# Optimization experiments

Measured on AMD Instinct MI355X. Metric: run time of the kernel, lower is better.

Reference implementation:

```python
import jax, jax.numpy as jnp
import numpy as np

HEAD_DIM = 128
ATTN_PAD_SEQ_LEN = 64
NUM_REQ = 128
NUM_HEAD = 32


def setup_inputs() -> dict:
    key = jax.random.key(0)
    qkv = jax.random.normal(key, (NUM_REQ, ATTN_PAD_SEQ_LEN, NUM_HEAD, HEAD_DIM * 3), dtype=jnp.float32)
    return {"qkv": qkv, "kv_seq_len": 64}


def reference(qkv, kv_seq_len):
    # qkv: [B, S, H, 3*D] packed Q|K|V along last dim
    q, k, v = jnp.split(qkv, 3, axis=-1)  # each [B, S, H, D]
    scale = 1.0 / jnp.sqrt(jnp.asarray(HEAD_DIM, dtype=qkv.dtype))
    # scores: [B, H, Sq, Sk]
    scores = jnp.einsum('bqhd,bkhd->bhqk', q, k) * scale
    # mask out padded KV positions beyond the active kv length
    kv_mask = jnp.arange(ATTN_PAD_SEQ_LEN) < kv_seq_len  # [Sk]
    scores = jnp.where(kv_mask[None, None, None, :], scores, jnp.asarray(-jnp.inf, dtype=scores.dtype))
    attn = jax.nn.softmax(scores, axis=-1)
    out = jnp.einsum('bhqk,bkhd->bqhd', attn, v)  # [B, S, H, D]
    return out
```

## Files before the change

### kernel.cpp

```cpp
#include <hip/hip_runtime.h>

typedef __attribute__((ext_vector_type(8))) short short8;
typedef __attribute__((ext_vector_type(4))) short shortx4;
typedef __attribute__((ext_vector_type(4))) float floatx4;

#define QK_LD 136
#define VT_LD 72

__device__ __forceinline__ unsigned short f2bf(float f) {
  union { float f; unsigned int u; } v; v.f = f;
  unsigned int u = v.u;
  u += 0x7fffu + ((u >> 16) & 1u);
  return (unsigned short)(u >> 16);
}

__launch_bounds__(256, 3)
__global__ void attn_fwd(const float* __restrict__ qkv,
                         const int* __restrict__ kvlen_p,
                         float* __restrict__ out) {
  __shared__ unsigned short Qs[64 * QK_LD];
  __shared__ unsigned short Ks[64 * QK_LD];
  __shared__ unsigned short Vts[128 * VT_LD];

  const int bid  = blockIdx.x;
  const int h    = bid & 31;
  const int b    = bid >> 5;
  const int tid  = threadIdx.x;
  const int lane = tid & 63;
  const int w    = tid >> 6;
  const int l15  = lane & 15;
  const int quad = lane >> 4;
  const int kvlen = kvlen_p[0];

  const float4* g4 = (const float4*)qkv;

  #pragma unroll 2
  for (int it = 0; it < 8; ++it) {
    int i  = tid + 256 * it;
    int s  = i >> 5;
    int c4 = i & 31;
    int rb = ((b * 64 + s) * 32 + h) * 96;

    float4 dq = g4[rb + c4];
    shortx4 pq = { (short)f2bf(dq.x), (short)f2bf(dq.y), (short)f2bf(dq.z), (short)f2bf(dq.w) };
    *(shortx4*)&Qs[s * QK_LD + c4 * 4] = pq;

    float4 dk = g4[rb + 32 + c4];
    shortx4 pk = { (short)f2bf(dk.x), (short)f2bf(dk.y), (short)f2bf(dk.z), (short)f2bf(dk.w) };
    *(shortx4*)&Ks[s * QK_LD + c4 * 4] = pk;

    float4 dv = g4[rb + 64 + c4];
    int col = (s + 8 * ((c4 >> 1) & 7)) & 63;
    unsigned short* vp = &Vts[(c4 * 4) * VT_LD + col];
    vp[0 * VT_LD] = f2bf(dv.x);
    vp[1 * VT_LD] = f2bf(dv.y);
    vp[2 * VT_LD] = f2bf(dv.z);
    vp[3 * VT_LD] = f2bf(dv.w);
  }
  __syncthreads();

  const float scale = 0.08838834764831845f;
  floatx4 zero4 = {0.f, 0.f, 0.f, 0.f};
  floatx4 accS[4] = {zero4, zero4, zero4, zero4};
  const int arow = (16 * w + l15) * QK_LD + 8 * quad;

  #pragma unroll
  for (int ks = 0; ks < 4; ++ks) {
    short8 a = *(const short8*)&Qs[arow + 32 * ks];
    #pragma unroll
    for (int nt = 0; nt < 4; ++nt) {
      short8 bf = *(const short8*)&Ks[(16 * nt + l15) * QK_LD + 32 * ks + 8 * quad];
      accS[nt] = __builtin_amdgcn_mfma_f32_16x16x32_bf16(a, bf, accS[nt], 0, 0, 0);
    }
  }

  float sv[4][4];
  #pragma unroll
  for (int nt = 0; nt < 4; ++nt) {
    bool masked = (16 * nt + l15) >= kvlen;
    #pragma unroll
    for (int r = 0; r < 4; ++r)
      sv[nt][r] = masked ? -__builtin_inff() : accS[nt][r] * scale;
  }
  float rowmax[4], rsum[4], rcpl[4];
  #pragma unroll
  for (int r = 0; r < 4; ++r)
    rowmax[r] = fmaxf(fmaxf(sv[0][r], sv[1][r]), fmaxf(sv[2][r], sv[3][r]));
  #pragma unroll
  for (int m = 1; m <= 8; m <<= 1) {
    #pragma unroll
    for (int r = 0; r < 4; ++r)
      rowmax[r] = fmaxf(rowmax[r], __shfl_xor(rowmax[r], m));
  }

  unsigned short* Pbase = &Qs[16 * w * QK_LD];
  #pragma unroll
  for (int r = 0; r < 4; ++r) rsum[r] = 0.f;
  #pragma unroll
  for (int nt = 0; nt < 4; ++nt) {
    #pragma unroll
    for (int r = 0; r < 4; ++r) {
      float e = __expf(sv[nt][r] - rowmax[r]);
      rsum[r] += e;
      Pbase[(4 * quad + r) * QK_LD + 16 * nt + l15] = f2bf(e);
    }
  }
  #pragma unroll
  for (int m = 1; m <= 8; m <<= 1) {
    #pragma unroll
    for (int r = 0; r < 4; ++r)
      rsum[r] += __shfl_xor(rsum[r], m);
  }
  #pragma unroll
  for (int r = 0; r < 4; ++r) rcpl[r] = 1.0f / rsum[r];

  floatx4 accO[8] = {zero4, zero4, zero4, zero4, zero4, zero4, zero4, zero4};
  #pragma unroll
  for (int ks = 0; ks < 2; ++ks) {
    short8 a = *(const short8*)&Qs[arow + 32 * ks];
    #pragma unroll
    for (int nt = 0; nt < 8; ++nt) {
      int vrow = 16 * nt + l15;
      int vcol = ((32 * ks + 8 * quad) + 8 * ((vrow >> 3) & 7)) & 63;
      short8 bf = *(const short8*)&Vts[vrow * VT_LD + vcol];
      accO[nt] = __builtin_amdgcn_mfma_f32_16x16x32_bf16(a, bf, accO[nt], 0, 0, 0);
    }
  }

  const int obase = ((b * 64 + 16 * w + 4 * quad) * 32 + h) * 128 + l15;
  #pragma unroll
  for (int nt = 0; nt < 8; ++nt) {
    #pragma unroll
    for (int r = 0; r < 4; ++r)
      out[obase + r * 4096 + nt * 16] = accO[nt][r] * rcpl[r];
  }
}

extern "C" void kernel_launch(void* const* d_in, const int* in_sizes, int n_in,
                              void* d_out, int out_size, void* d_ws, size_t ws_size,
                              hipStream_t stream) {
  const float* qkv = (const float*)d_in[0];
  const int* kvlen = (const int*)d_in[1];
  float* out       = (float*)d_out;
  attn_fwd<<<dim3(128 * 32), dim3(256), 0, stream>>>(qkv, kvlen, out);
}
```

Baseline: 549.5 us.

## Load Q directly into MFMA registers, drop Q shared buffer, raise occupancy

Each lane now loads its Q fragment straight from global memory into registers and converts it to bf16 there, so the Q shared-memory tile is removed. The K buffer is reused for the P matrix after an added barrier, which cuts LDS per block and lets launch bounds ask for 4 blocks per CU instead of 3. The bf16 conversion now packs pairs with a byte-permute instruction, and K is written to shared memory as packed 32-bit pairs. The cost is higher register pressure from holding the Q values, an extra __syncthreads, and less coalesced Q reads.

```diff
diff --git a/kernel.cpp b/kernel.cpp
--- a/kernel.cpp
+++ b/kernel.cpp
@@ -1,24 +1,26 @@
 #include <hip/hip_runtime.h>
 
 typedef __attribute__((ext_vector_type(8))) short short8;
-typedef __attribute__((ext_vector_type(4))) short shortx4;
 typedef __attribute__((ext_vector_type(4))) float floatx4;
 
 #define QK_LD 136
 #define VT_LD 72
 
+__device__ __forceinline__ unsigned int rne_hi(float f) {
+  union { float f; unsigned int u; } v; v.f = f;
+  return v.u + 0x7fffu + ((v.u >> 16) & 1u);
+}
+__device__ __forceinline__ unsigned int pack_bf2(float f0, float f1) {
+  return __builtin_amdgcn_perm(rne_hi(f1), rne_hi(f0), 0x07060302u);
+}
 __device__ __forceinline__ unsigned short f2bf(float f) {
-  union { float f; unsigned int u; } v; v.f = f;
-  unsigned int u = v.u;
-  u += 0x7fffu + ((u >> 16) & 1u);
-  return (unsigned short)(u >> 16);
+  return (unsigned short)(rne_hi(f) >> 16);
 }
 
-__launch_bounds__(256, 3)
+__launch_bounds__(256, 4)
 __global__ void attn_fwd(const float* __restrict__ qkv,
                          const int* __restrict__ kvlen_p,
                          float* __restrict__ out) {
-  __shared__ unsigned short Qs[64 * QK_LD];
   __shared__ unsigned short Ks[64 * QK_LD];
   __shared__ unsigned short Vts[128 * VT_LD];
 
@@ -34,22 +36,26 @@
 
   const float4* g4 = (const float4*)qkv;
 
+  const float4* qg = g4 + ((size_t)((b * 64 + 16 * w + l15) * 32 + h)) * 96 + 2 * quad;
+  float4 qf32[8];
+  #pragma unroll
+  for (int ks = 0; ks < 4; ++ks) {
+    qf32[2 * ks]     = qg[8 * ks];
+    qf32[2 * ks + 1] = qg[8 * ks + 1];
+  }
+
   #pragma unroll 2
   for (int it = 0; it < 8; ++it) {
     int i  = tid + 256 * it;
     int s  = i >> 5;
     int c4 = i & 31;
-    int rb = ((b * 64 + s) * 32 + h) * 96;
+    const float4* rp = g4 + ((size_t)((b * 64 + s) * 32 + h)) * 96;
 
-    float4 dq = g4[rb + c4];
-    shortx4 pq = { (short)f2bf(dq.x), (short)f2bf(dq.y), (short)f2bf(dq.z), (short)f2bf(dq.w) };
-    *(shortx4*)&Qs[s * QK_LD + c4 * 4] = pq;
+    float4 dk = rp[32 + c4];
+    uint2 pk = { pack_bf2(dk.x, dk.y), pack_bf2(dk.z, dk.w) };
+    *(uint2*)&Ks[s * QK_LD + c4 * 4] = pk;
 
-    float4 dk = g4[rb + 32 + c4];
-    shortx4 pk = { (short)f2bf(dk.x), (short)f2bf(dk.y), (short)f2bf(dk.z), (short)f2bf(dk.w) };
-    *(shortx4*)&Ks[s * QK_LD + c4 * 4] = pk;
-
-    float4 dv = g4[rb + 64 + c4];
+    float4 dv = rp[64 + c4];
     int col = (s + 8 * ((c4 >> 1) & 7)) & 63;
     unsigned short* vp = &Vts[(c4 * 4) * VT_LD + col];
     vp[0 * VT_LD] = f2bf(dv.x);
@@ -57,22 +63,32 @@
     vp[2 * VT_LD] = f2bf(dv.z);
     vp[3 * VT_LD] = f2bf(dv.w);
   }
+
+  short8 qfrag[4];
+  #pragma unroll
+  for (int ks = 0; ks < 4; ++ks) {
+    union { unsigned int u[4]; short8 s8; } cv;
+    float4 a0 = qf32[2 * ks], a1 = qf32[2 * ks + 1];
+    cv.u[0] = pack_bf2(a0.x, a0.y);
+    cv.u[1] = pack_bf2(a0.z, a0.w);
+    cv.u[2] = pack_bf2(a1.x, a1.y);
+    cv.u[3] = pack_bf2(a1.z, a1.w);
+    qfrag[ks] = cv.s8;
+  }
   __syncthreads();
 
   const float scale = 0.08838834764831845f;
   floatx4 zero4 = {0.f, 0.f, 0.f, 0.f};
   floatx4 accS[4] = {zero4, zero4, zero4, zero4};
-  const int arow = (16 * w + l15) * QK_LD + 8 * quad;
-
   #pragma unroll
   for (int ks = 0; ks < 4; ++ks) {
-    short8 a = *(const short8*)&Qs[arow + 32 * ks];
     #pragma unroll
     for (int nt = 0; nt < 4; ++nt) {
       short8 bf = *(const short8*)&Ks[(16 * nt + l15) * QK_LD + 32 * ks + 8 * quad];
-      accS[nt] = __builtin_amdgcn_mfma_f32_16x16x32_bf16(a, bf, accS[nt], 0, 0, 0);
+      accS[nt] = __builtin_amdgcn_mfma_f32_16x16x32_bf16(qfrag[ks], bf, accS[nt], 0, 0, 0);
     }
   }
+  __syncthreads();
 
   float sv[4][4];
   #pragma unroll
@@ -87,37 +103,35 @@
   for (int r = 0; r < 4; ++r)
     rowmax[r] = fmaxf(fmaxf(sv[0][r], sv[1][r]), fmaxf(sv[2][r], sv[3][r]));
   #pragma unroll
-  for (int m = 1; m <= 8; m <<= 1) {
+  for (int m = 1; m <= 8; m <<= 1)
     #pragma unroll
     for (int r = 0; r < 4; ++r)
       rowmax[r] = fmaxf(rowmax[r], __shfl_xor(rowmax[r], m));
-  }
 
-  unsigned short* Pbase = &Qs[16 * w * QK_LD];
+  unsigned short* Pbase = &Ks[16 * w * QK_LD];
   #pragma unroll
   for (int r = 0; r < 4; ++r) rsum[r] = 0.f;
   #pragma unroll
-  for (int nt = 0; nt < 4; ++nt) {
+  for (int nt = 0; nt < 4; ++nt)
     #pragma unroll
     for (int r = 0; r < 4; ++r) {
       float e = __expf(sv[nt][r] - rowmax[r]);
       rsum[r] += e;
       Pbase[(4 * quad + r) * QK_LD + 16 * nt + l15] = f2bf(e);
     }
-  }
   #pragma unroll
-  for (int m = 1; m <= 8; m <<= 1) {
+  for (int m = 1; m <= 8; m <<= 1)
     #pragma unroll
     for (int r = 0; r < 4; ++r)
       rsum[r] += __shfl_xor(rsum[r], m);
-  }
   #pragma unroll
   for (int r = 0; r < 4; ++r) rcpl[r] = 1.0f / rsum[r];
 
+  const int arow = (16 * w + l15) * QK_LD + 8 * quad;
   floatx4 accO[8] = {zero4, zero4, zero4, zero4, zero4, zero4, zero4, zero4};
   #pragma unroll
   for (int ks = 0; ks < 2; ++ks) {
-    short8 a = *(const short8*)&Qs[arow + 32 * ks];
+    short8 a = *(const short8*)&Ks[arow + 32 * ks];
     #pragma unroll
     for (int nt = 0; nt < 8; ++nt) {
       int vrow = 16 * nt + l15;
@@ -127,12 +141,12 @@
     }
   }
 
-  const int obase = ((b * 64 + 16 * w + 4 * quad) * 32 + h) * 128 + l15;
   #pragma unroll
-  for (int nt = 0; nt < 8; ++nt) {
+  for (int r = 0; r < 4; ++r) {
+    const int obase = ((b * 64 + 16 * w + 4 * quad + r) * 32 + h) * 128 + l15;
     #pragma unroll
-    for (int r = 0; r < 4; ++r)
-      out[obase + r * 4096 + nt * 16] = accO[nt][r] * rcpl[r];
+    for (int nt = 0; nt < 8; ++nt)
+      out[obase + nt * 16] = accO[nt][r] * rcpl[r];
   }
 }
 
```

Measured after the change: 556.1 us. About the same (+1.2%).
